# Performance work log

Measured on AMD Instinct MI355X. Metric: run time of the kernel, lower is better.

Reference implementation:

```python
import jax, jax.numpy as jnp
import numpy as np
import math

LOG2PI = math.log(2.0 * math.pi)

def _silu(x):
    return x * jax.nn.sigmoid(x)

def _gru(x, W_ih, W_hh, b_ih, b_hh):
    # x: [B,T,X]; torch nn.GRU single layer, batch_first
    B = x.shape[0]
    H = W_hh.shape[1]
    gi_all = jnp.einsum('btx,gx->btg', x, W_ih) + b_ih  # [B,T,3H] input gates precomputed
    def step(h, gi):
        gh = h @ W_hh.T + b_hh
        i_r, i_z, i_n = jnp.split(gi, 3, axis=-1)
        h_r, h_z, h_n = jnp.split(gh, 3, axis=-1)
        r = jax.nn.sigmoid(i_r + h_r)
        z = jax.nn.sigmoid(i_z + h_z)
        n = jnp.tanh(i_n + r * h_n)
        h_new = (1.0 - z) * n + z * h
        return h_new, h_new
    h0 = jnp.zeros((B, H), x.dtype)
    h_last, h_seq = jax.lax.scan(step, h0, jnp.swapaxes(gi_all, 0, 1))
    return jnp.swapaxes(h_seq, 0, 1), h_last  # [B,T,H], [B,H]

def _A_Q(kappa, sigma, dt):
    A = jnp.exp(-kappa * dt)
    two_k_dt = 2.0 * kappa * dt
    small = (two_k_dt < 1e-6).astype(dt.dtype)
    Q_exact = sigma ** 2 * (1.0 - jnp.exp(-two_k_dt)) / jnp.maximum(2.0 * kappa, 1e-12)
    Q_taylor = sigma ** 2 * dt * (1.0 - kappa * dt + two_k_dt ** 2 / 6.0)
    Q = small * Q_taylor + (1.0 - small) * Q_exact
    return A, Q

def _ou_posterior(m0, s0, mu_k, A_k, Q_k, eps0, eps):
    B, Tm1, C = mu_k.shape
    c0 = m0 + s0 * eps0  # [B,C]
    s0c = jnp.maximum(s0, 1e-12)
    log_q0 = -0.5 * (((c0 - m0) / s0c) ** 2 + 2.0 * jnp.log(s0c) + LOG2PI).sum(-1)
    noise = eps * jnp.sqrt(jnp.maximum(Q_k, 1e-12))
    b = (1.0 - A_k) * mu_k + noise
    Phi_prefix = jnp.cumprod(A_k, axis=1)  # [B,T-1,C]
    Phi_full = jnp.concatenate([jnp.ones((B, 1, C), mu_k.dtype), Phi_prefix], axis=1)
    denom = jnp.maximum(Phi_full[:, 1:, :], 1e-20)
    s = b / denom
    S_full = jnp.concatenate([jnp.zeros((B, 1, C), mu_k.dtype), jnp.cumsum(s, axis=1)], axis=1)
    c = Phi_full * (c0[:, None, :] + S_full)  # [B,T,C]
    mean_trans = mu_k + A_k * (c[:, :-1, :] - mu_k)
    var_trans = jnp.maximum(Q_k, 1e-12)
    log_q_trans = -0.5 * ((c[:, 1:, :] - mean_trans) ** 2 / var_trans + jnp.log(var_trans) + LOG2PI)
    log_q = log_q0 + log_q_trans.sum(-1).sum(-1)
    return c, log_q

def reference(x, t, eps0, eps, W_ih, W_hh, b_ih, b_hh, Wi1, bi1, Wi2, bi2, Ws1, bs1, Ws2, bs2, Ws3, bs3):
    B, T, _ = x.shape
    h_seq, h_global = _gru(x, W_ih, W_hh, b_ih, b_hh)
    # soft time attention, temperature = 1.0
    delta = t[:, :, None, 0] - t[:, None, :, 0]  # [B,T,T]
    logits = -(T * delta) ** 2  # / tau^2 with tau=1
    w = jax.nn.softmax(logits, axis=-1)
    attn = jnp.einsum('bkj,bjh->bkh', w, h_seq)
    # init head
    h0_ctx = h_global + attn[:, 0, :]
    hi = _silu(h0_ctx @ Wi1.T + bi1)
    m0, logs0 = jnp.split(hi @ Wi2.T + bi2, 2, axis=-1)
    s0 = jax.nn.softplus(logs0) + 1e-6
    # step head on ctx[:, :-1]
    ctx = jnp.concatenate([h_global[:, None, :] + attn, t], axis=-1)[:, :-1, :]
    hs = _silu(ctx @ Ws1.T + bs1)
    hs = _silu(hs @ Ws2.T + bs2)
    params = hs @ Ws3.T + bs3
    mu_k, logk_k, logs_k = jnp.split(params, 3, axis=-1)
    kappa_k = jax.nn.softplus(logk_k) + 1e-6
    sigma_k = jax.nn.softplus(logs_k) + 1e-6
    dt = jnp.maximum(t[:, 1:, :] - t[:, :-1, :], 1e-6)
    A_k, Q_k = _A_Q(kappa_k, sigma_k, dt)
    c, log_q = _ou_posterior(m0, s0, mu_k, A_k, Q_k, eps0, eps)
    return c, log_q

def setup_inputs() -> dict:
    B, T, X, H, C = 8, 2048, 64, 256, 32
    key = jax.random.key(0)
    ks = jax.random.split(key, 16)
    def w(k, shape, scale=0.02):
        return (scale * jax.random.normal(k, shape)).astype(jnp.float32)
    x = jax.random.normal(ks[0], (B, T, X), dtype=jnp.float32)
    t = jnp.sort(jax.random.uniform(ks[1], (B, T, 1), dtype=jnp.float32), axis=1)
    eps0 = jax.random.normal(ks[2], (B, C), dtype=jnp.float32)
    eps = jax.random.normal(ks[3], (B, T - 1, C), dtype=jnp.float32)
    return {
        'x': x, 't': t, 'eps0': eps0, 'eps': eps,
        'W_ih': w(ks[4], (3 * H, X)), 'W_hh': w(ks[5], (3 * H, H)),
        'b_ih': jnp.zeros((3 * H,), jnp.float32), 'b_hh': jnp.zeros((3 * H,), jnp.float32),
        'Wi1': w(ks[6], (H, H)), 'bi1': jnp.zeros((H,), jnp.float32),
        'Wi2': w(ks[7], (2 * C, H)), 'bi2': jnp.zeros((2 * C,), jnp.float32),
        'Ws1': w(ks[8], (H, H + 1)), 'bs1': jnp.zeros((H,), jnp.float32),
        'Ws2': w(ks[9], (H, H)), 'bs2': jnp.zeros((H,), jnp.float32),
        'Ws3': w(ks[10], (3 * C, H)), 'bs3': jnp.zeros((3 * C,), jnp.float32),
    }
```

## Files before the change

### kernel.cpp

```cpp
#include <hip/hip_runtime.h>
#include <hip/hip_fp16.h>

#define LOG2PI_F 1.8378770664093453f

typedef _Float16 hf2_t __attribute__((ext_vector_type(2)));

#if defined(__has_builtin)
#  if __has_builtin(__builtin_amdgcn_fdot2)
#    define USE_FDOT2 1
#  endif
#endif
#ifndef USE_FDOT2
#  define USE_FDOT2 0
#endif

__device__ __forceinline__ float fdot2(unsigned int a, unsigned int b, float c) {
#if USE_FDOT2
  return __builtin_amdgcn_fdot2(__builtin_bit_cast(hf2_t, a),
                                __builtin_bit_cast(hf2_t, b), c, false);
#else
  __half2 ha = __builtin_bit_cast(__half2, a);
  __half2 hb = __builtin_bit_cast(__half2, b);
  float2 fa = __half22float2(ha);
  float2 fb = __half22float2(hb);
  return c + fa.x * fb.x + fa.y * fb.y;
#endif
}

__device__ __forceinline__ unsigned int packh2(float lo, float hi) {
  unsigned int l = (unsigned int)__half_as_ushort(__float2half(lo));
  unsigned int h = (unsigned int)__half_as_ushort(__float2half(hi));
  return (h << 16) | l;
}

__device__ __forceinline__ float sigmoid_f(float x) { return 1.f / (1.f + __expf(-x)); }
__device__ __forceinline__ float silu_f(float x) { return x * sigmoid_f(x); }
__device__ __forceinline__ float softplus_f(float x) {
  return fmaxf(x, 0.f) + log1pf(__expf(-fabsf(x)));
}
__device__ __forceinline__ float tanh_f(float x) {
  float ax = fabsf(x);
  float e = __expf(2.f * ax);
  return copysignf(1.f - 2.f / (e + 1.f), x);
}

__global__ void transpose_k(const float* __restrict__ in, float* __restrict__ out,
                            int R, int C) {
  int i = blockIdx.x * 256 + threadIdx.x;
  if (i < R * C) {
    int r = i / C, c = i % C;
    out[c * R + r] = in[i];
  }
}

__global__ void whh_pack(const float* __restrict__ W, unsigned int* __restrict__ WpkT) {
  int i = blockIdx.x * 256 + threadIdx.x;
  if (i < 98304) {
    int d = i / 768, g = i % 768;
    float lo = W[g * 256 + 2 * d];
    float hi = W[g * 256 + 2 * d + 1];
    WpkT[i] = packh2(lo, hi);
  }
}

__global__ void gi_gemm(const float* __restrict__ x, const float* __restrict__ WT,
                        const float* __restrict__ bih, float* __restrict__ gi) {
  int m0 = blockIdx.x * 8;
  int g = threadIdx.x;
  __shared__ float xs[8][64];
  for (int i = g; i < 512; i += 256) xs[i >> 6][i & 63] = x[m0 * 64 + i];
  __syncthreads();
  float b0 = bih[g], b1 = bih[g + 256], b2 = bih[g + 512];
  float a0[8], a1[8], a2[8];
#pragma unroll
  for (int r = 0; r < 8; r++) { a0[r] = b0; a1[r] = b1; a2[r] = b2; }
  for (int k = 0; k < 64; k++) {
    const float* w = WT + k * 768;
    float w0 = w[g], w1 = w[g + 256], w2 = w[g + 512];
#pragma unroll
    for (int r = 0; r < 8; r++) {
      float xv = xs[r][k];
      a0[r] = fmaf(w0, xv, a0[r]);
      a1[r] = fmaf(w1, xv, a1[r]);
      a2[r] = fmaf(w2, xv, a2[r]);
    }
  }
#pragma unroll
  for (int r = 0; r < 8; r++) {
    float* o = gi + (m0 + r) * 768;
    o[g] = a0[r];
    o[g + 256] = a1[r];
    o[g + 512] = a2[r];
  }
}

__global__ __launch_bounds__(768, 3) void gru_kernel(
    const unsigned int* __restrict__ WpkT,
    const float* __restrict__ gi,
    const float* __restrict__ bhh,
    float* __restrict__ h_seq)
{
  const int b = blockIdx.x;
  const int g = threadIdx.x;

  uint4 w[32];
#pragma unroll
  for (int i = 0; i < 32; i++) {
    int d = 4 * i;
    w[i] = make_uint4(WpkT[(d + 0) * 768 + g], WpkT[(d + 1) * 768 + g],
                      WpkT[(d + 2) * 768 + g], WpkT[(d + 3) * 768 + g]);
  }

  __shared__ __align__(16) unsigned int hpk[2][128];
  __shared__ float als[1024];
  if (g < 128) hpk[0][g] = 0u;

  const float bb = bhh[g];
  float h = 0.f;
  const float* gib = gi + b * 2048 * 768;
  float* hsb = h_seq + b * 2048 * 256;
  float gcur = gib[g];
  __syncthreads();

  for (int t = 0; t < 2048; t++) {
    float gnext = gib[min(t + 1, 2047) * 768 + g];

    const uint4* hp = (const uint4*)hpk[t & 1];
    float a = bb;
#pragma unroll
    for (int i = 0; i < 32; i++) {
      uint4 hv = hp[i];
      a = fdot2(w[i].x, hv.x, a);
      a = fdot2(w[i].y, hv.y, a);
      a = fdot2(w[i].z, hv.z, a);
      a = fdot2(w[i].w, hv.w, a);
    }
    if (g < 512) {
      als[g] = a + gcur;
    } else {
      als[g] = a;
      als[g + 256] = gcur;
    }
    __syncthreads();

    if (g < 256) {
      float rv = sigmoid_f(als[g]);
      float zv = sigmoid_f(als[256 + g]);
      float nv = tanh_f(als[768 + g] + rv * als[512 + g]);
      float hn = (1.f - zv) * nv + zv * h;
      h = hn;
      hsb[t * 256 + g] = hn;
      float other = __shfl_xor(hn, 1);
      if ((g & 1) == 0) hpk[(t + 1) & 1][g >> 1] = packh2(hn, other);
    }
    gcur = gnext;
    __syncthreads();
  }
}

#define AW 80
__global__ void attn_kernel(const float* __restrict__ h_seq, const float* __restrict__ t,
                            float* __restrict__ ctx) {
  const int blk = blockIdx.x;
  const int b = blk >> 7;
  const int k0 = (blk & 127) << 4;
  const int tid = threadIdx.x;

  __shared__ __align__(16) float ewT[176][16];
  __shared__ float ts[176];
  __shared__ float tks[16];
  __shared__ float rden[16];

  const float* tb = t + b * 2048;
  if (tid < 176) {
    int j = k0 - AW + tid;
    ts[tid] = tb[min(max(j, 0), 2047)];
  }
  if (tid < 16) tks[tid] = tb[k0 + tid];
  __syncthreads();

  for (int p = tid; p < 176 * 16; p += 256) {
    int kk = p & 15, jr = p >> 4;
    int j = k0 - AW + jr;
    float d = 2048.f * (tks[kk] - ts[jr]);
    float e = (j >= 0 && j < 2048) ? __expf(-d * d) : 0.f;
    ewT[jr][kk] = e;
  }
  __syncthreads();

  if (tid < 16) {
    float s = 0.f;
    for (int jr = 0; jr < 176; jr++) s += ewT[jr][tid];
    rden[tid] = 1.f / s;
  }
  __syncthreads();

  float acc[16];
#pragma unroll
  for (int kk = 0; kk < 16; kk++) acc[kk] = 0.f;

  const float* hb = h_seq + b * 2048 * 256;
  for (int jr = 0; jr < 176; jr++) {
    int j = min(max(k0 - AW + jr, 0), 2047);
    float hv = hb[j * 256 + tid];
    const float4* e4 = (const float4*)ewT[jr];
    float4 e0 = e4[0], e1 = e4[1], e2 = e4[2], e3 = e4[3];
    acc[0] = fmaf(e0.x, hv, acc[0]);   acc[1] = fmaf(e0.y, hv, acc[1]);
    acc[2] = fmaf(e0.z, hv, acc[2]);   acc[3] = fmaf(e0.w, hv, acc[3]);
    acc[4] = fmaf(e1.x, hv, acc[4]);   acc[5] = fmaf(e1.y, hv, acc[5]);
    acc[6] = fmaf(e1.z, hv, acc[6]);   acc[7] = fmaf(e1.w, hv, acc[7]);
    acc[8] = fmaf(e2.x, hv, acc[8]);   acc[9] = fmaf(e2.y, hv, acc[9]);
    acc[10] = fmaf(e2.z, hv, acc[10]); acc[11] = fmaf(e2.w, hv, acc[11]);
    acc[12] = fmaf(e3.x, hv, acc[12]); acc[13] = fmaf(e3.y, hv, acc[13]);
    acc[14] = fmaf(e3.z, hv, acc[14]); acc[15] = fmaf(e3.w, hv, acc[15]);
  }

  float hg = hb[2047 * 256 + tid];
  float* cb = ctx + (b * 2048 + k0) * 256 + tid;
#pragma unroll
  for (int kk = 0; kk < 16; kk++) cb[kk * 256] = hg + acc[kk] * rden[kk];
}

__global__ void init_head(const float* __restrict__ ctx, const float* __restrict__ WT1,
                          const float* __restrict__ bi1, const float* __restrict__ WT2,
                          const float* __restrict__ bi2, const float* __restrict__ eps0,
                          float* __restrict__ m0s0, float* __restrict__ lq0) {
  int b = blockIdx.x;
  int g = threadIdx.x;
  __shared__ float xs[256], his[256], ms[64], red[32];
  xs[g] = ctx[(b * 2048) * 256 + g];
  __syncthreads();
  float acc = bi1[g];
#pragma unroll 8
  for (int k = 0; k < 256; k++) acc = fmaf(WT1[k * 256 + g], xs[k], acc);
  his[g] = silu_f(acc);
  __syncthreads();
  if (g < 64) {
    float a2 = bi2[g];
#pragma unroll 8
    for (int k = 0; k < 256; k++) a2 = fmaf(WT2[k * 64 + g], his[k], a2);
    float v = (g < 32) ? a2 : (softplus_f(a2) + 1e-6f);
    m0s0[b * 64 + g] = v;
    ms[g] = v;
  }
  __syncthreads();
  if (g < 32) {
    float m = ms[g], s = ms[32 + g];
    float c0 = m + s * eps0[b * 32 + g];
    float sc = fmaxf(s, 1e-12f);
    float z = (c0 - m) / sc;
    red[g] = z * z + 2.f * __logf(sc) + LOG2PI_F;
  }
  __syncthreads();
  if (g == 0) {
    float s = 0.f;
    for (int i = 0; i < 32; i++) s += red[i];
    lq0[b] = -0.5f * s;
  }
}

__global__ void head_layer(const float* __restrict__ A, const float* __restrict__ WT,
                           const float* __restrict__ bias, const float* __restrict__ wext,
                           const float* __restrict__ tvec, float* __restrict__ C,
                           int N, int act) {
  int m0 = blockIdx.x * 8;
  int g = threadIdx.x;
  __shared__ __align__(16) float As[8][256];
#pragma unroll
  for (int r = 0; r < 8; r++) As[r][g] = A[(m0 + r) * 256 + g];
  __syncthreads();
  if (g < N) {
    float b0 = bias[g];
    float acc[8] = {b0, b0, b0, b0, b0, b0, b0, b0};
    for (int k4 = 0; k4 < 64; k4++) {
      const float* w = WT + (k4 * 4) * N + g;
      float w0v = w[0], w1v = w[N], w2v = w[2 * N], w3v = w[3 * N];
#pragma unroll
      for (int r = 0; r < 8; r++) {
        float4 xv = *(const float4*)(&As[r][k4 * 4]);
        acc[r] = fmaf(w0v, xv.x, acc[r]);
        acc[r] = fmaf(w1v, xv.y, acc[r]);
        acc[r] = fmaf(w2v, xv.z, acc[r]);
        acc[r] = fmaf(w3v, xv.w, acc[r]);
      }
    }
#pragma unroll
    for (int r = 0; r < 8; r++) {
      float a = acc[r];
      if (wext) a = fmaf(tvec[m0 + r], wext[g], a);
      if (act) a = silu_f(a);
      C[(m0 + r) * N + g] = a;
    }
  }
}

__global__ __launch_bounds__(1024) void ou_kernel(
    const float* __restrict__ params, const float* __restrict__ t,
    const float* __restrict__ eps, const float* __restrict__ eps0,
    const float* __restrict__ m0s0, const float* __restrict__ lq0,
    float* __restrict__ out) {
  const int b = blockIdx.x;
  const int c = threadIdx.x & 31;
  const int s = threadIdx.x >> 5;
  const int k0 = s * 64;
  const int k1 = min(k0 + 64, 2047);
  const float* tb = t + b * 2048;

  __shared__ float Ps[32][33], Ss[32][33], Cs[32][33], lqs[32][33];

  float P = 1.f, S = 0.f, lq = 0.f;
  for (int k = k0; k < k1; k++) {
    const float* pr = params + (b * 2048 + k) * 96;
    float mu = pr[c];
    float kap = softplus_f(pr[32 + c]) + 1e-6f;
    float sg = softplus_f(pr[64 + c]) + 1e-6f;
    float dt = fmaxf(tb[k + 1] - tb[k], 1e-6f);
    float A = __expf(-kap * dt);
    float tkd = 2.f * kap * dt;
    float Qe = sg * sg * (1.f - A * A) / fmaxf(2.f * kap, 1e-12f);
    float kd = kap * dt;
    float Qt = sg * sg * dt * (1.f - kd + tkd * tkd * (1.f / 6.f));
    float var = fmaxf((tkd < 1e-6f) ? Qt : Qe, 1e-12f);
    float e = eps[(b * 2047 + k) * 32 + c];
    float d = mu * (1.f - A) + e * sqrtf(var);
    S = fmaf(A, S, d);
    P *= A;
    lq += e * e + __logf(var) + LOG2PI_F;
  }
  Ps[c][s] = P;
  Ss[c][s] = S;
  lqs[c][s] = lq;
  __syncthreads();

  if (s == 0) {
    float m0v = m0s0[b * 64 + c];
    float s0v = m0s0[b * 64 + 32 + c];
    float cc = fmaf(s0v, eps0[b * 32 + c], m0v);
    out[(b * 2048) * 32 + c] = cc;
    float lqt = 0.f;
    for (int i = 0; i < 32; i++) {
      Cs[c][i] = cc;
      cc = fmaf(Ps[c][i], cc, Ss[c][i]);
      lqt += lqs[c][i];
    }
    for (int off = 16; off >= 1; off >>= 1) lqt += __shfl_down(lqt, off, 32);
    if (c == 0) out[8 * 2048 * 32 + b] = lq0[b] - 0.5f * lqt;
  }
  __syncthreads();

  float cc = Cs[c][s];
  for (int k = k0; k < k1; k++) {
    const float* pr = params + (b * 2048 + k) * 96;
    float mu = pr[c];
    float kap = softplus_f(pr[32 + c]) + 1e-6f;
    float sg = softplus_f(pr[64 + c]) + 1e-6f;
    float dt = fmaxf(tb[k + 1] - tb[k], 1e-6f);
    float A = __expf(-kap * dt);
    float tkd = 2.f * kap * dt;
    float Qe = sg * sg * (1.f - A * A) / fmaxf(2.f * kap, 1e-12f);
    float kd = kap * dt;
    float Qt = sg * sg * dt * (1.f - kd + tkd * tkd * (1.f / 6.f));
    float var = fmaxf((tkd < 1e-6f) ? Qt : Qe, 1e-12f);
    float e = eps[(b * 2047 + k) * 32 + c];
    float d = mu * (1.f - A) + e * sqrtf(var);
    cc = fmaf(A, cc, d);
    out[(b * 2048 + k + 1) * 32 + c] = cc;
  }
}

extern "C" void kernel_launch(void* const* d_in, const int* in_sizes, int n_in,
                              void* d_out, int out_size, void* d_ws, size_t ws_size,
                              hipStream_t stream) {
  (void)in_sizes; (void)n_in; (void)out_size; (void)ws_size;
  const float* x    = (const float*)d_in[0];
  const float* t    = (const float*)d_in[1];
  const float* eps0 = (const float*)d_in[2];
  const float* eps  = (const float*)d_in[3];
  const float* W_ih = (const float*)d_in[4];
  const float* W_hh = (const float*)d_in[5];
  const float* b_ih = (const float*)d_in[6];
  const float* b_hh = (const float*)d_in[7];
  const float* Wi1  = (const float*)d_in[8];
  const float* bi1  = (const float*)d_in[9];
  const float* Wi2  = (const float*)d_in[10];
  const float* bi2  = (const float*)d_in[11];
  const float* Ws1  = (const float*)d_in[12];
  const float* bs1  = (const float*)d_in[13];
  const float* Ws2  = (const float*)d_in[14];
  const float* bs2  = (const float*)d_in[15];
  const float* Ws3  = (const float*)d_in[16];
  const float* bs3  = (const float*)d_in[17];
  float* out = (float*)d_out;
  float* ws = (float*)d_ws;

  float*        WT_ih = ws + 0;
  unsigned int* WpkT  = (unsigned int*)(ws + 49152);
  float*        WT1   = ws + 147456;
  float*        WT2   = ws + 212992;
  float*        WTs1  = ws + 229376;
  float*        WTs2  = ws + 295168;
  float*        WTs3  = ws + 360704;
  float*        m0s0  = ws + 385280;
  float*        lq0   = ws + 385792;
  float*        gi    = ws + 385800;
  float*        h_seq = gi + 12582912;
  float*        ctx   = h_seq + 4194304;
  float*        hs1    = gi;
  float*        hs2    = gi + 4194304;
  float*        params = gi + 8388608;

  transpose_k<<<(768 * 64 + 255) / 256, 256, 0, stream>>>(W_ih, WT_ih, 768, 64);
  transpose_k<<<(256 * 256 + 255) / 256, 256, 0, stream>>>(Wi1, WT1, 256, 256);
  transpose_k<<<(64 * 256 + 255) / 256, 256, 0, stream>>>(Wi2, WT2, 64, 256);
  transpose_k<<<(256 * 257 + 255) / 256, 256, 0, stream>>>(Ws1, WTs1, 256, 257);
  transpose_k<<<(256 * 256 + 255) / 256, 256, 0, stream>>>(Ws2, WTs2, 256, 256);
  transpose_k<<<(96 * 256 + 255) / 256, 256, 0, stream>>>(Ws3, WTs3, 96, 256);
  whh_pack<<<384, 256, 0, stream>>>(W_hh, WpkT);

  gi_gemm<<<2048, 256, 0, stream>>>(x, WT_ih, b_ih, gi);
  gru_kernel<<<8, 768, 0, stream>>>(WpkT, gi, b_hh, h_seq);
  attn_kernel<<<1024, 256, 0, stream>>>(h_seq, t, ctx);
  init_head<<<8, 256, 0, stream>>>(ctx, WT1, bi1, WT2, bi2, eps0, m0s0, lq0);
  head_layer<<<2048, 256, 0, stream>>>(ctx, WTs1, bs1, WTs1 + 256 * 256, t, hs1, 256, 1);
  head_layer<<<2048, 256, 0, stream>>>(hs1, WTs2, bs2, nullptr, nullptr, hs2, 256, 1);
  head_layer<<<2048, 256, 0, stream>>>(hs2, WTs3, bs3, nullptr, nullptr, params, 96, 0);
  ou_kernel<<<8, 1024, 0, stream>>>(params, t, eps, eps0, m0s0, lq0, out);
}
```

Measured before the change: 3.155 ms.

## Restructure GRU step to 512 threads with shuffle-based gate exchange and one barrier

The GRU recurrence now runs with 512 threads per batch element instead of 768. Each thread pair owns one hidden unit: one thread computes the r gate and the other the z gate, and each thread computes half of the n-gate dot product. The r/z values, n partials and input-gate terms are combined with lane shuffles, which removes the LDS staging array and one __syncthreads per timestep. To match this mapping, the W_hh packing and the gi output layout are interleaved. The cost is more weight registers per thread (48 uint4) and extra shuffle traffic, which could lower occupancy or cause spills.

```diff
diff --git a/kernel.cpp b/kernel.cpp
--- a/kernel.cpp
+++ b/kernel.cpp
@@ -53,13 +53,20 @@
   }
 }
 
-__global__ void whh_pack(const float* __restrict__ W, unsigned int* __restrict__ WpkT) {
+__global__ void whh_pack2(const float* __restrict__ W, unsigned int* __restrict__ Wpk2) {
   int i = blockIdx.x * 256 + threadIdx.x;
-  if (i < 98304) {
-    int d = i / 768, g = i % 768;
-    float lo = W[g * 256 + 2 * d];
-    float hi = W[g * 256 + 2 * d + 1];
-    WpkT[i] = packh2(lo, hi);
+  if (i < 512 * 192) {
+    int t = i / 192, d = i % 192;
+    int k = t >> 1;
+    int row, p0;
+    if (d < 128) {
+      row = (t & 1) ? (256 + k) : k;
+      p0 = 2 * d;
+    } else {
+      row = 512 + k;
+      p0 = 2 * (d - 128) + ((t & 1) ? 128 : 0);
+    }
+    Wpk2[i] = packh2(W[row * 256 + p0], W[row * 256 + p0 + 1]);
   }
 }
 
@@ -88,72 +95,83 @@
 #pragma unroll
   for (int r = 0; r < 8; r++) {
     float* o = gi + (m0 + r) * 768;
-    o[g] = a0[r];
-    o[g + 256] = a1[r];
-    o[g + 512] = a2[r];
-  }
-}
-
-__global__ __launch_bounds__(768, 3) void gru_kernel(
-    const unsigned int* __restrict__ WpkT,
+    o[2 * g] = a0[r];
+    o[2 * g + 1] = a1[r];
+    o[512 + g] = a2[r];
+  }
+}
+
+__global__ __launch_bounds__(512, 2) void gru_kernel(
+    const unsigned int* __restrict__ Wpk2,
     const float* __restrict__ gi,
     const float* __restrict__ bhh,
     float* __restrict__ h_seq)
 {
   const int b = blockIdx.x;
-  const int g = threadIdx.x;
-
-  uint4 w[32];
-#pragma unroll
-  for (int i = 0; i < 32; i++) {
-    int d = 4 * i;
-    w[i] = make_uint4(WpkT[(d + 0) * 768 + g], WpkT[(d + 1) * 768 + g],
-                      WpkT[(d + 2) * 768 + g], WpkT[(d + 3) * 768 + g]);
-  }
+  const int tid = threadIdx.x;
+  const int k = tid >> 1;
+  const int odd = tid & 1;
+
+  uint4 wp[32], wn[16];
+  const uint4* wsrc = (const uint4*)(Wpk2 + tid * 192);
+#pragma unroll
+  for (int i = 0; i < 32; i++) wp[i] = wsrc[i];
+#pragma unroll
+  for (int i = 0; i < 16; i++) wn[i] = wsrc[32 + i];
 
   __shared__ __align__(16) unsigned int hpk[2][128];
-  __shared__ float als[1024];
-  if (g < 128) hpk[0][g] = 0u;
-
-  const float bb = bhh[g];
+  if (tid < 128) hpk[0][tid] = 0u;
+
+  const float bbp = bhh[odd ? (256 + k) : k];
+  const float bbn = bhh[512 + k];
   float h = 0.f;
   const float* gib = gi + b * 2048 * 768;
   float* hsb = h_seq + b * 2048 * 256;
-  float gcur = gib[g];
+  float gp = gib[tid];
+  float gn = odd ? 0.f : gib[512 + k];
   __syncthreads();
 
   for (int t = 0; t < 2048; t++) {
-    float gnext = gib[min(t + 1, 2047) * 768 + g];
+    const float* gnx = gib + min(t + 1, 2047) * 768;
+    float gp_n = gnx[tid];
+    float gn_n = odd ? 0.f : gnx[512 + k];
 
     const uint4* hp = (const uint4*)hpk[t & 1];
-    float a = bb;
+    const uint4* hq = hp + (odd ? 16 : 0);
+    float ap0 = bbp + gp, ap1 = 0.f, an = 0.f;
 #pragma unroll
     for (int i = 0; i < 32; i++) {
       uint4 hv = hp[i];
-      a = fdot2(w[i].x, hv.x, a);
-      a = fdot2(w[i].y, hv.y, a);
-      a = fdot2(w[i].z, hv.z, a);
-      a = fdot2(w[i].w, hv.w, a);
-    }
-    if (g < 512) {
-      als[g] = a + gcur;
-    } else {
-      als[g] = a;
-      als[g + 256] = gcur;
-    }
-    __syncthreads();
-
-    if (g < 256) {
-      float rv = sigmoid_f(als[g]);
-      float zv = sigmoid_f(als[256 + g]);
-      float nv = tanh_f(als[768 + g] + rv * als[512 + g]);
-      float hn = (1.f - zv) * nv + zv * h;
-      h = hn;
-      hsb[t * 256 + g] = hn;
-      float other = __shfl_xor(hn, 1);
-      if ((g & 1) == 0) hpk[(t + 1) & 1][g >> 1] = packh2(hn, other);
-    }
-    gcur = gnext;
+      ap0 = fdot2(wp[i].x, hv.x, ap0);
+      ap0 = fdot2(wp[i].y, hv.y, ap0);
+      ap1 = fdot2(wp[i].z, hv.z, ap1);
+      ap1 = fdot2(wp[i].w, hv.w, ap1);
+    }
+#pragma unroll
+    for (int i = 0; i < 16; i++) {
+      uint4 hv = hq[i];
+      an = fdot2(wn[i].x, hv.x, an);
+      an = fdot2(wn[i].y, hv.y, an);
+      an = fdot2(wn[i].z, hv.z, an);
+      an = fdot2(wn[i].w, hv.w, an);
+    }
+
+    float sg = sigmoid_f(ap0 + ap1);
+    float so = __shfl_xor(sg, 1);
+    float r = odd ? so : sg;
+    float z = odd ? sg : so;
+    float ant = an + __shfl_xor(an, 1);
+    float gno = __shfl_xor(gn, 1);
+    float gin = odd ? gno : gn;
+    float nv = tanh_f(gin + r * (ant + bbn));
+    h = (1.f - z) * nv + z * h;
+
+    if (!odd) hsb[t * 256 + k] = h;
+    float hnb = __shfl_xor(h, 2);
+    if ((tid & 3) == 0) hpk[(t + 1) & 1][tid >> 2] = packh2(h, hnb);
+
+    gp = gp_n;
+    gn = gn_n;
     __syncthreads();
   }
 }
@@ -394,7 +412,7 @@
   float* ws = (float*)d_ws;
 
   float*        WT_ih = ws + 0;
-  unsigned int* WpkT  = (unsigned int*)(ws + 49152);
+  unsigned int* Wpk2  = (unsigned int*)(ws + 49152);
   float*        WT1   = ws + 147456;
   float*        WT2   = ws + 212992;
   float*        WTs1  = ws + 229376;
@@ -415,10 +433,10 @@
   transpose_k<<<(256 * 257 + 255) / 256, 256, 0, stream>>>(Ws1, WTs1, 256, 257);
   transpose_k<<<(256 * 256 + 255) / 256, 256, 0, stream>>>(Ws2, WTs2, 256, 256);
   transpose_k<<<(96 * 256 + 255) / 256, 256, 0, stream>>>(Ws3, WTs3, 96, 256);
-  whh_pack<<<384, 256, 0, stream>>>(W_hh, WpkT);
+  whh_pack2<<<(512 * 192 + 255) / 256, 256, 0, stream>>>(W_hh, Wpk2);
 
   gi_gemm<<<2048, 256, 0, stream>>>(x, WT_ih, b_ih, gi);
-  gru_kernel<<<8, 768, 0, stream>>>(WpkT, gi, b_hh, h_seq);
+  gru_kernel<<<8, 512, 0, stream>>>(Wpk2, gi, b_hh, h_seq);
   attn_kernel<<<1024, 256, 0, stream>>>(h_seq, t, ctx);
   init_head<<<8, 256, 0, stream>>>(ctx, WT1, bi1, WT2, bi2, eps0, m0s0, lq0);
   head_layer<<<2048, 256, 0, stream>>>(ctx, WTs1, bs1, WTs1 + 256 * 256, t, hs1, 256, 1);
```

New measurement: 4.041 ms. 1.28x slower.

## Restructure GRU recurrence so 4-lane groups own one hidden unit with shuffle reduction

Applied to the files above, without the earlier changes.

The GRU kernel now runs 1024 threads per sequence, with each group of 4 lanes computing all three gate dot products for one hidden unit over a quarter of the hidden vector. Partial sums are combined with xor shuffles, so the shared-memory gate exchange and one __syncthreads per step are gone. W_hh is repacked to match, with a rotated read order intended to avoid LDS bank conflicts, and gi is written interleaved per unit. The intent is to shorten the serial per-timestep latency. In exchange it uses more threads and a different register footprint (24 uint4 of weights per thread).

```diff
diff --git a/kernel.cpp b/kernel.cpp
--- a/kernel.cpp
+++ b/kernel.cpp
@@ -53,13 +53,16 @@
   }
 }
 
-__global__ void whh_pack(const float* __restrict__ W, unsigned int* __restrict__ WpkT) {
-  int i = blockIdx.x * 256 + threadIdx.x;
-  if (i < 98304) {
-    int d = i / 768, g = i % 768;
-    float lo = W[g * 256 + 2 * d];
-    float hi = W[g * 256 + 2 * d + 1];
-    WpkT[i] = packh2(lo, hi);
+__global__ void whh_pack3(const float* __restrict__ W, unsigned int* __restrict__ Wpk3) {
+  int idx = blockIdx.x * 256 + threadIdx.x;
+  if (idx < 1024 * 96) {
+    int tid = idx / 96, c = idx % 96;
+    int q = tid & 3, k = tid >> 2;
+    int g = c / 32, r32 = c % 32;
+    int i = r32 / 4, e = r32 % 4;
+    int p = 32 * q + 4 * ((i + 2 * q) & 7) + e;
+    int row = g * 256 + k;
+    Wpk3[idx] = packh2(W[row * 256 + 2 * p], W[row * 256 + 2 * p + 1]);
   }
 }
 
@@ -88,70 +91,79 @@
 #pragma unroll
   for (int r = 0; r < 8; r++) {
     float* o = gi + (m0 + r) * 768;
-    o[g] = a0[r];
-    o[g + 256] = a1[r];
-    o[g + 512] = a2[r];
-  }
-}
-
-__global__ __launch_bounds__(768, 3) void gru_kernel(
-    const unsigned int* __restrict__ WpkT,
+    o[3 * g + 0] = a0[r];
+    o[3 * g + 1] = a1[r];
+    o[3 * g + 2] = a2[r];
+  }
+}
+
+__global__ __launch_bounds__(1024, 4) void gru_kernel(
+    const unsigned int* __restrict__ Wpk3,
     const float* __restrict__ gi,
     const float* __restrict__ bhh,
     float* __restrict__ h_seq)
 {
   const int b = blockIdx.x;
-  const int g = threadIdx.x;
-
-  uint4 w[32];
-#pragma unroll
-  for (int i = 0; i < 32; i++) {
-    int d = 4 * i;
-    w[i] = make_uint4(WpkT[(d + 0) * 768 + g], WpkT[(d + 1) * 768 + g],
-                      WpkT[(d + 2) * 768 + g], WpkT[(d + 3) * 768 + g]);
-  }
+  const int tid = threadIdx.x;
+  const int k = tid >> 2;
+  const int q = tid & 3;
+
+  uint4 wq[24];
+  const uint4* wsrc = (const uint4*)(Wpk3 + tid * 96);
+#pragma unroll
+  for (int i = 0; i < 24; i++) wq[i] = wsrc[i];
 
   __shared__ __align__(16) unsigned int hpk[2][128];
-  __shared__ float als[1024];
-  if (g < 128) hpk[0][g] = 0u;
-
-  const float bb = bhh[g];
+  if (tid < 128) hpk[0][tid] = 0u;
+
+  const float bb = (q < 3) ? bhh[q * 256 + k] : 0.f;
   float h = 0.f;
   const float* gib = gi + b * 2048 * 768;
   float* hsb = h_seq + b * 2048 * 256;
-  float gcur = gib[g];
+  const int gidx = 3 * k + q;
+  float gcur = (q < 3) ? gib[gidx] : 0.f;
   __syncthreads();
 
   for (int t = 0; t < 2048; t++) {
-    float gnext = gib[min(t + 1, 2047) * 768 + g];
-
-    const uint4* hp = (const uint4*)hpk[t & 1];
-    float a = bb;
-#pragma unroll
-    for (int i = 0; i < 32; i++) {
-      uint4 hv = hp[i];
-      a = fdot2(w[i].x, hv.x, a);
-      a = fdot2(w[i].y, hv.y, a);
-      a = fdot2(w[i].z, hv.z, a);
-      a = fdot2(w[i].w, hv.w, a);
-    }
-    if (g < 512) {
-      als[g] = a + gcur;
-    } else {
-      als[g] = a;
-      als[g + 256] = gcur;
-    }
-    __syncthreads();
-
-    if (g < 256) {
-      float rv = sigmoid_f(als[g]);
-      float zv = sigmoid_f(als[256 + g]);
-      float nv = tanh_f(als[768 + g] + rv * als[512 + g]);
-      float hn = (1.f - zv) * nv + zv * h;
-      h = hn;
-      hsb[t * 256 + g] = hn;
-      float other = __shfl_xor(hn, 1);
-      if ((g & 1) == 0) hpk[(t + 1) & 1][g >> 1] = packh2(hn, other);
+    float gnext = (q < 3) ? gib[min(t + 1, 2047) * 768 + gidx] : 0.f;
+
+    const uint4* hb = (const uint4*)hpk[t & 1];
+    float ar = (q == 0) ? (gcur + bb) : 0.f;
+    float az = (q == 1) ? (gcur + bb) : 0.f;
+    float an = (q == 2) ? bb : 0.f;
+    float ai = (q == 2) ? gcur : 0.f;
+#pragma unroll
+    for (int i = 0; i < 8; i++) {
+      uint4 hv = hb[8 * q + ((i + 2 * q) & 7)];
+      uint4 wr = wq[i], wz = wq[8 + i], wn = wq[16 + i];
+      ar = fdot2(wr.x, hv.x, ar);
+      ar = fdot2(wr.y, hv.y, ar);
+      ar = fdot2(wr.z, hv.z, ar);
+      ar = fdot2(wr.w, hv.w, ar);
+      az = fdot2(wz.x, hv.x, az);
+      az = fdot2(wz.y, hv.y, az);
+      az = fdot2(wz.z, hv.z, az);
+      az = fdot2(wz.w, hv.w, az);
+      an = fdot2(wn.x, hv.x, an);
+      an = fdot2(wn.y, hv.y, an);
+      an = fdot2(wn.z, hv.z, an);
+      an = fdot2(wn.w, hv.w, an);
+    }
+#pragma unroll
+    for (int off = 1; off <= 2; off <<= 1) {
+      ar += __shfl_xor(ar, off);
+      az += __shfl_xor(az, off);
+      an += __shfl_xor(an, off);
+      ai += __shfl_xor(ai, off);
+    }
+    float r = sigmoid_f(ar);
+    float z = sigmoid_f(az);
+    float nv = tanh_f(ai + r * an);
+    h = (1.f - z) * nv + z * h;
+
+    if (q == 0) {
+      hsb[t * 256 + k] = h;
+      ((__half*)hpk[(t + 1) & 1])[k] = __float2half(h);
     }
     gcur = gnext;
     __syncthreads();
@@ -394,7 +406,7 @@
   float* ws = (float*)d_ws;
 
   float*        WT_ih = ws + 0;
-  unsigned int* WpkT  = (unsigned int*)(ws + 49152);
+  unsigned int* Wpk3  = (unsigned int*)(ws + 49152);
   float*        WT1   = ws + 147456;
   float*        WT2   = ws + 212992;
   float*        WTs1  = ws + 229376;
@@ -415,10 +427,10 @@
   transpose_k<<<(256 * 257 + 255) / 256, 256, 0, stream>>>(Ws1, WTs1, 256, 257);
   transpose_k<<<(256 * 256 + 255) / 256, 256, 0, stream>>>(Ws2, WTs2, 256, 256);
   transpose_k<<<(96 * 256 + 255) / 256, 256, 0, stream>>>(Ws3, WTs3, 96, 256);
-  whh_pack<<<384, 256, 0, stream>>>(W_hh, WpkT);
+  whh_pack3<<<(1024 * 96 + 255) / 256, 256, 0, stream>>>(W_hh, Wpk3);
 
   gi_gemm<<<2048, 256, 0, stream>>>(x, WT_ih, b_ih, gi);
-  gru_kernel<<<8, 768, 0, stream>>>(WpkT, gi, b_hh, h_seq);
+  gru_kernel<<<8, 1024, 0, stream>>>(Wpk3, gi, b_hh, h_seq);
   attn_kernel<<<1024, 256, 0, stream>>>(h_seq, t, ctx);
   init_head<<<8, 256, 0, stream>>>(ctx, WT1, bi1, WT2, bi2, eps0, m0s0, lq0);
   head_layer<<<2048, 256, 0, stream>>>(ctx, WTs1, bs1, WTs1 + 256 * 256, t, hs1, 256, 1);
```

Result: slower. 3.680 ms (+16.6%).

## Use MFMA 16x16x32 f16 for GRU recurrent matvec with prepacked weights

Applied to the files above, without the earlier changes.

The per-step W_hh·h product in the sequential GRU loop now runs on MFMA matrix instructions instead of per-thread fdot2 chains. Weights are prepacked into the MFMA A-operand layout, and the broadcast h vector serves as the B operand. Only one column of each output tile is written back to LDS. The r and z hidden biases are folded into the precomputed input gates. The change targets the latency-bound 2048-step recurrence, but it computes 15 unused columns per MFMA and adds layout complexity.

```diff
diff --git a/kernel.cpp b/kernel.cpp
--- a/kernel.cpp
+++ b/kernel.cpp
@@ -3,29 +3,8 @@
 
 #define LOG2PI_F 1.8378770664093453f
 
-typedef _Float16 hf2_t __attribute__((ext_vector_type(2)));
-
-#if defined(__has_builtin)
-#  if __has_builtin(__builtin_amdgcn_fdot2)
-#    define USE_FDOT2 1
-#  endif
-#endif
-#ifndef USE_FDOT2
-#  define USE_FDOT2 0
-#endif
-
-__device__ __forceinline__ float fdot2(unsigned int a, unsigned int b, float c) {
-#if USE_FDOT2
-  return __builtin_amdgcn_fdot2(__builtin_bit_cast(hf2_t, a),
-                                __builtin_bit_cast(hf2_t, b), c, false);
-#else
-  __half2 ha = __builtin_bit_cast(__half2, a);
-  __half2 hb = __builtin_bit_cast(__half2, b);
-  float2 fa = __half22float2(ha);
-  float2 fb = __half22float2(hb);
-  return c + fa.x * fb.x + fa.y * fb.y;
-#endif
-}
+typedef _Float16 hf8_t __attribute__((ext_vector_type(8)));
+typedef float f32x4_t __attribute__((ext_vector_type(4)));
 
 __device__ __forceinline__ unsigned int packh2(float lo, float hi) {
   unsigned int l = (unsigned int)__half_as_ushort(__float2half(lo));
@@ -53,24 +32,32 @@
   }
 }
 
-__global__ void whh_pack(const float* __restrict__ W, unsigned int* __restrict__ WpkT) {
-  int i = blockIdx.x * 256 + threadIdx.x;
-  if (i < 98304) {
-    int d = i / 768, g = i % 768;
-    float lo = W[g * 256 + 2 * d];
-    float hi = W[g * 256 + 2 * d + 1];
-    WpkT[i] = packh2(lo, hi);
+__global__ void whh_mfma_pack(const float* __restrict__ W, unsigned int* __restrict__ Wmf) {
+  int idx = blockIdx.x * 256 + threadIdx.x;
+  if (idx < 98304) {
+    int d = idx & 3;
+    int u4 = idx >> 2;
+    int lane = u4 & 63;
+    int rem = u4 >> 6;
+    int kt = rem & 7;
+    int mt = rem >> 3;
+    int row = 16 * mt + (lane & 15);
+    int col = 32 * kt + 8 * (lane >> 4) + 2 * d;
+    Wmf[idx] = packh2(W[row * 256 + col], W[row * 256 + col + 1]);
   }
 }
 
 __global__ void gi_gemm(const float* __restrict__ x, const float* __restrict__ WT,
-                        const float* __restrict__ bih, float* __restrict__ gi) {
+                        const float* __restrict__ bih, const float* __restrict__ bhh,
+                        float* __restrict__ gi) {
   int m0 = blockIdx.x * 8;
   int g = threadIdx.x;
   __shared__ float xs[8][64];
   for (int i = g; i < 512; i += 256) xs[i >> 6][i & 63] = x[m0 * 64 + i];
   __syncthreads();
-  float b0 = bih[g], b1 = bih[g + 256], b2 = bih[g + 512];
+  float b0 = bih[g] + bhh[g];
+  float b1 = bih[g + 256] + bhh[g + 256];
+  float b2 = bih[g + 512];
   float a0[8], a1[8], a2[8];
 #pragma unroll
   for (int r = 0; r < 8; r++) { a0[r] = b0; a1[r] = b1; a2[r] = b2; }
@@ -95,65 +82,85 @@
 }
 
 __global__ __launch_bounds__(768, 3) void gru_kernel(
-    const unsigned int* __restrict__ WpkT,
+    const uint4* __restrict__ Wmf,
     const float* __restrict__ gi,
     const float* __restrict__ bhh,
     float* __restrict__ h_seq)
 {
   const int b = blockIdx.x;
-  const int g = threadIdx.x;
-
-  uint4 w[32];
-#pragma unroll
-  for (int i = 0; i < 32; i++) {
-    int d = 4 * i;
-    w[i] = make_uint4(WpkT[(d + 0) * 768 + g], WpkT[(d + 1) * 768 + g],
-                      WpkT[(d + 2) * 768 + g], WpkT[(d + 3) * 768 + g]);
-  }
+  const int tid = threadIdx.x;
+  const int w = tid >> 6;
+  const int lane = tid & 63;
+
+  uint4 wA[32];
+#pragma unroll
+  for (int i = 0; i < 32; i++) wA[i] = Wmf[(w * 32 + i) * 64 + lane];
 
   __shared__ __align__(16) unsigned int hpk[2][128];
-  __shared__ float als[1024];
-  if (g < 128) hpk[0][g] = 0u;
-
-  const float bb = bhh[g];
-  float h = 0.f;
+  __shared__ __align__(16) float als[768];
+  if (tid < 128) hpk[0][tid] = 0u;
+
   const float* gib = gi + b * 2048 * 768;
   float* hsb = h_seq + b * 2048 * 256;
-  float gcur = gib[g];
+
+  float h = 0.f, bn = 0.f, gr = 0.f, gz = 0.f, gn = 0.f;
+  if (tid < 256) {
+    bn = bhh[512 + tid];
+    gr = gib[tid];
+    gz = gib[256 + tid];
+    gn = gib[512 + tid];
+  }
   __syncthreads();
 
   for (int t = 0; t < 2048; t++) {
-    float gnext = gib[min(t + 1, 2047) * 768 + g];
-
-    const uint4* hp = (const uint4*)hpk[t & 1];
-    float a = bb;
-#pragma unroll
-    for (int i = 0; i < 32; i++) {
-      uint4 hv = hp[i];
-      a = fdot2(w[i].x, hv.x, a);
-      a = fdot2(w[i].y, hv.y, a);
-      a = fdot2(w[i].z, hv.z, a);
-      a = fdot2(w[i].w, hv.w, a);
-    }
-    if (g < 512) {
-      als[g] = a + gcur;
-    } else {
-      als[g] = a;
-      als[g + 256] = gcur;
+    float grn = 0.f, gzn = 0.f, gnn = 0.f;
+    if (tid < 256) {
+      const float* gnx = gib + min(t + 1, 2047) * 768;
+      grn = gnx[tid];
+      gzn = gnx[256 + tid];
+      gnn = gnx[512 + tid];
+    }
+
+    const char* hb = (const char*)(hpk[t & 1]) + 16 * (lane >> 4);
+    f32x4_t a0 = {0.f, 0.f, 0.f, 0.f}, a1 = a0, a2 = a0, a3 = a0;
+    uint4 hc = *(const uint4*)(hb);
+    uint4 hn = *(const uint4*)(hb + 64);
+#pragma unroll
+    for (int kt = 0; kt < 8; kt++) {
+      hf8_t bf = __builtin_bit_cast(hf8_t, hc);
+      a0 = __builtin_amdgcn_mfma_f32_16x16x32_f16(
+          __builtin_bit_cast(hf8_t, wA[kt]), bf, a0, 0, 0, 0);
+      a1 = __builtin_amdgcn_mfma_f32_16x16x32_f16(
+          __builtin_bit_cast(hf8_t, wA[8 + kt]), bf, a1, 0, 0, 0);
+      a2 = __builtin_amdgcn_mfma_f32_16x16x32_f16(
+          __builtin_bit_cast(hf8_t, wA[16 + kt]), bf, a2, 0, 0, 0);
+      a3 = __builtin_amdgcn_mfma_f32_16x16x32_f16(
+          __builtin_bit_cast(hf8_t, wA[24 + kt]), bf, a3, 0, 0, 0);
+      hc = hn;
+      if (kt < 6) hn = *(const uint4*)(hb + 64 * (kt + 2));
+    }
+    if ((lane & 15) == 0) {
+      int rbase = 64 * w + 4 * (lane >> 4);
+      *(f32x4_t*)&als[rbase] = a0;
+      *(f32x4_t*)&als[rbase + 16] = a1;
+      *(f32x4_t*)&als[rbase + 32] = a2;
+      *(f32x4_t*)&als[rbase + 48] = a3;
     }
     __syncthreads();
 
-    if (g < 256) {
-      float rv = sigmoid_f(als[g]);
-      float zv = sigmoid_f(als[256 + g]);
-      float nv = tanh_f(als[768 + g] + rv * als[512 + g]);
-      float hn = (1.f - zv) * nv + zv * h;
-      h = hn;
-      hsb[t * 256 + g] = hn;
-      float other = __shfl_xor(hn, 1);
-      if ((g & 1) == 0) hpk[(t + 1) & 1][g >> 1] = packh2(hn, other);
-    }
-    gcur = gnext;
+    if (tid < 256) {
+      float rv = sigmoid_f(als[tid] + gr);
+      float zv = sigmoid_f(als[256 + tid] + gz);
+      float nv = tanh_f(gn + rv * (als[512 + tid] + bn));
+      float hnew = (1.f - zv) * nv + zv * h;
+      h = hnew;
+      hsb[t * 256 + tid] = hnew;
+      float other = __shfl_xor(hnew, 1);
+      if ((tid & 1) == 0) hpk[(t + 1) & 1][tid >> 1] = packh2(hnew, other);
+    }
+    gr = grn;
+    gz = gzn;
+    gn = gnn;
     __syncthreads();
   }
 }
@@ -394,7 +401,7 @@
   float* ws = (float*)d_ws;
 
   float*        WT_ih = ws + 0;
-  unsigned int* WpkT  = (unsigned int*)(ws + 49152);
+  unsigned int* Wmf   = (unsigned int*)(ws + 49152);
   float*        WT1   = ws + 147456;
   float*        WT2   = ws + 212992;
   float*        WTs1  = ws + 229376;
@@ -415,10 +422,10 @@
   transpose_k<<<(256 * 257 + 255) / 256, 256, 0, stream>>>(Ws1, WTs1, 256, 257);
   transpose_k<<<(256 * 256 + 255) / 256, 256, 0, stream>>>(Ws2, WTs2, 256, 256);
   transpose_k<<<(96 * 256 + 255) / 256, 256, 0, stream>>>(Ws3, WTs3, 96, 256);
-  whh_pack<<<384, 256, 0, stream>>>(W_hh, WpkT);
-
-  gi_gemm<<<2048, 256, 0, stream>>>(x, WT_ih, b_ih, gi);
-  gru_kernel<<<8, 768, 0, stream>>>(WpkT, gi, b_hh, h_seq);
+  whh_mfma_pack<<<384, 256, 0, stream>>>(W_hh, Wmf);
+
+  gi_gemm<<<2048, 256, 0, stream>>>(x, WT_ih, b_ih, b_hh, gi);
+  gru_kernel<<<8, 768, 0, stream>>>((const uint4*)Wmf, gi, b_hh, h_seq);
   attn_kernel<<<1024, 256, 0, stream>>>(h_seq, t, ctx);
   init_head<<<8, 256, 0, stream>>>(ctx, WT1, bi1, WT2, bi2, eps0, m0s0, lq0);
   head_layer<<<2048, 256, 0, stream>>>(ctx, WTs1, bs1, WTs1 + 256 * 256, t, hs1, 256, 1);
```

Result: slower. 3.657 ms (+15.9%).
